# Kernel optimization log

Hardware: AMD Instinct MI355X
Metric: run time of the kernel (lower is better)

The kernel has to match this reference:

```python
import jax, jax.numpy as jnp
import numpy as np

B, S, D = 2, 2048, 1024
H = 16
HD = D // H
MLP = 4096
EPS = 1e-5


def _layernorm(x, g, b):
    mu = jnp.mean(x, axis=-1, keepdims=True)
    var = jnp.mean(jnp.square(x - mu), axis=-1, keepdims=True)
    return (x - mu) * jax.lax.rsqrt(var + EPS) * g + b


def setup_inputs() -> dict:
    key = jax.random.key(0)
    ks = jax.random.split(key, 16)
    sd = 0.02
    return {
        "x": jax.random.normal(ks[0], (B, S, D), jnp.float32),
        "dis_attn_mask": jax.random.normal(ks[1], (B, S, S), jnp.float32) * 0.1,
        "cls_attn_mask": jax.random.normal(ks[2], (B, S, S), jnp.float32) * 0.1,
        "wq": jax.random.normal(ks[3], (D, D), jnp.float32) * sd,
        "bq": jnp.zeros((D,), jnp.float32),
        "wk": jax.random.normal(ks[4], (D, D), jnp.float32) * sd,
        "bk": jnp.zeros((D,), jnp.float32),
        "wv": jax.random.normal(ks[5], (D, D), jnp.float32) * sd,
        "bv": jnp.zeros((D,), jnp.float32),
        "ln1_g": jnp.ones((D,), jnp.float32),
        "ln1_b": jnp.zeros((D,), jnp.float32),
        "ln2_g": jnp.ones((D,), jnp.float32),
        "ln2_b": jnp.zeros((D,), jnp.float32),
        "w1": jax.random.normal(ks[6], (D, MLP), jnp.float32) * sd,
        "b1": jnp.zeros((MLP,), jnp.float32),
        "w2": jax.random.normal(ks[7], (MLP, D), jnp.float32) * sd,
        "b2": jnp.zeros((D,), jnp.float32),
    }


def reference(x, dis_attn_mask, cls_attn_mask, wq, bq, wk, bk, wv, bv,
              ln1_g, ln1_b, ln2_g, ln2_b, w1, b1, w2, b2):
    res = x
    h = _layernorm(x, ln1_g, ln1_b)
    q = h @ wq + bq
    k = h @ wk + bk
    v = h @ wv + bv
    # NOTE: original torch code uses .view(B, H, S, HD) on a contiguous
    # [B, S, D] tensor (no transpose); row-major reshape reproduces this.
    q = q.reshape(B, H, S, HD)
    k = k.reshape(B, H, S, HD)
    v = v.reshape(B, H, S, HD)
    w = jnp.einsum('bhsd,bhtd->bhst', q, k) * (HD ** -0.5)
    w = w + dis_attn_mask[:, None] + cls_attn_mask[:, None]
    w = jax.nn.softmax(w, axis=-1)
    h_attn = jnp.einsum('bhst,bhtd->bhsd', w, v).reshape(B, S, D)
    h = h_attn + res
    h = _layernorm(h, ln2_g, ln2_b)
    res2 = h
    h = jax.nn.gelu(h @ w1 + b1, approximate=False) @ w2 + b2
    return h + res2
```

## Files before the change

kernel.cpp:

```cpp
#include <hip/hip_runtime.h>
#include <hip/hip_bf16.h>
#include <math.h>

#define BB 2
#define SS 2048
#define DD 1024
#define HH 16
#define MLPD 4096

typedef __attribute__((ext_vector_type(8))) short bf16x8;
typedef __attribute__((ext_vector_type(4))) float f32x4;
typedef __attribute__((ext_vector_type(4))) unsigned short us4;

static __device__ __forceinline__ float fast_exp2(float x) {
#if __has_builtin(__builtin_amdgcn_exp2f)
  return __builtin_amdgcn_exp2f(x);
#else
  return exp2f(x);
#endif
}
static __device__ __forceinline__ float fast_rcp(float x) {
#if __has_builtin(__builtin_amdgcn_rcpf)
  return __builtin_amdgcn_rcpf(x);
#else
  return 1.0f / x;
#endif
}

static __device__ __forceinline__ unsigned short f2bf(float f) {
  union { float f; unsigned int u; } v; v.f = f;
  unsigned int r = v.u + 0x7fffu + ((v.u >> 16) & 1u);
  return (unsigned short)(r >> 16);
}
static __device__ __forceinline__ float bf2f(unsigned short b) {
  return __uint_as_float(((unsigned int)b) << 16);
}

static __device__ __forceinline__ float gelu_f(float x) {
  float u = x * x;
  float z = x * fmaf(u, 0.0713548162f, 1.59576912f);
  float e = fast_exp2(z * -1.44269504f);
  return x * fast_rcp(1.0f + e);
}

static __device__ __forceinline__ int swz(int row) {
  return (row & 3) ^ ((row >> 2) & 3);
}

static __device__ __forceinline__ void async16(const unsigned short* g, unsigned short* l) {
  __builtin_amdgcn_global_load_lds(
      (const __attribute__((address_space(1))) unsigned int*)g,
      (__attribute__((address_space(3))) unsigned int*)l, 16, 0, 0);
}

__global__ __launch_bounds__(256) void transpose_to_bf16(
    const float* __restrict__ src, unsigned short* __restrict__ dst,
    int K, int N) {
  __shared__ float tile[32][33];
  int t = threadIdx.x;
  int c = t & 31, rl = t >> 5;
  int bx = blockIdx.x, by = blockIdx.y;
#pragma unroll
  for (int i = 0; i < 4; ++i) {
    int row = rl * 4 + i;
    tile[row][c] = src[(size_t)(by * 32 + row) * N + bx * 32 + c];
  }
  __syncthreads();
#pragma unroll
  for (int i = 0; i < 4; ++i) {
    int n = rl * 4 + i;
    dst[(size_t)(bx * 32 + n) * K + by * 32 + c] = f2bf(tile[c][n]);
  }
}

__global__ __launch_bounds__(256) void transpose_qkv(
    const float* __restrict__ wq, const float* __restrict__ wk,
    const float* __restrict__ wv, unsigned short* __restrict__ dst) {
  __shared__ float tile[32][33];
  const float* src = blockIdx.z == 0 ? wq : blockIdx.z == 1 ? wk : wv;
  unsigned short* d = dst + (size_t)blockIdx.z * 1024 * 1024;
  int t = threadIdx.x;
  int c = t & 31, rl = t >> 5;
  int bx = blockIdx.x, by = blockIdx.y;
#pragma unroll
  for (int i = 0; i < 4; ++i) {
    int row = rl * 4 + i;
    tile[row][c] = src[(size_t)(by * 32 + row) * DD + bx * 32 + c];
  }
  __syncthreads();
#pragma unroll
  for (int i = 0; i < 4; ++i) {
    int n = rl * 4 + i;
    d[(size_t)(bx * 32 + n) * DD + by * 32 + c] = f2bf(tile[c][n]);
  }
}

__global__ __launch_bounds__(256) void concat_bias(
    const float* __restrict__ bq, const float* __restrict__ bk,
    const float* __restrict__ bv, float* __restrict__ dst) {
  int i = blockIdx.x * 256 + threadIdx.x;
  if (i < 1024) dst[i] = bq[i];
  else if (i < 2048) dst[i] = bk[i - 1024];
  else if (i < 3072) dst[i] = bv[i - 2048];
}

__global__ __launch_bounds__(256) void mask_prep2(
    const float* __restrict__ dis, const float* __restrict__ cls,
    unsigned short* __restrict__ cmP) {
  int qt = blockIdx.x, wave = blockIdx.y, b = blockIdx.z;
  int tid = threadIdx.x;
  int ktg = tid >> 6, lane = tid & 63;
  int g = lane >> 4, c16 = lane & 15;
  const float* db = dis + (size_t)b * SS * SS;
  const float* cb = cls + (size_t)b * SS * SS;
  unsigned short* ob =
      cmP + ((((size_t)b * 16 + qt) * 8 + wave) * 32) * 64 * 16;
  int row0 = qt * 128 + wave * 16 + g * 4;
#pragma unroll
  for (int i = 0; i < 8; ++i) {
    int kt = ktg * 8 + i;
    int col0 = kt * 64 + c16;
    short v[16];
#pragma unroll
    for (int t = 0; t < 4; ++t)
#pragma unroll
      for (int r = 0; r < 4; ++r) {
        size_t idx = (size_t)(row0 + r) * SS + col0 + t * 16;
        v[t * 4 + r] = (short)f2bf((db[idx] + cb[idx]) * 8.0f);
      }
    unsigned short* o = ob + ((size_t)kt * 64 + lane) * 16;
    *(bf16x8*)(o) = *(bf16x8*)&v[0];
    *(bf16x8*)(o + 8) = *(bf16x8*)&v[8];
  }
}

template <bool BF_IN, bool ADD>
__global__ __launch_bounds__(256) void ln_bf16(
    const void* __restrict__ in, const float* __restrict__ add,
    const float* __restrict__ g, const float* __restrict__ beta,
    unsigned short* __restrict__ out) {
  int row = blockIdx.x;
  int t = threadIdx.x;
  float x[4];
  if (BF_IN) {
    us4 b4 = *(const us4*)((const unsigned short*)in + (size_t)row * DD + t * 4);
#pragma unroll
    for (int i = 0; i < 4; ++i) x[i] = bf2f(b4[i]);
  } else {
    float4 f4 = *(const float4*)((const float*)in + (size_t)row * DD + t * 4);
    x[0] = f4.x; x[1] = f4.y; x[2] = f4.z; x[3] = f4.w;
  }
  if (ADD) {
    float4 a4 = *(const float4*)(add + (size_t)row * DD + t * 4);
    x[0] += a4.x; x[1] += a4.y; x[2] += a4.z; x[3] += a4.w;
  }
  float s1 = x[0] + x[1] + x[2] + x[3];
  float s2 = x[0] * x[0] + x[1] * x[1] + x[2] * x[2] + x[3] * x[3];
#pragma unroll
  for (int off = 32; off > 0; off >>= 1) {
    s1 += __shfl_down(s1, off);
    s2 += __shfl_down(s2, off);
  }
  __shared__ float sa[4], sb[4];
  int wid = t >> 6;
  if ((t & 63) == 0) { sa[wid] = s1; sb[wid] = s2; }
  __syncthreads();
  s1 = sa[0] + sa[1] + sa[2] + sa[3];
  s2 = sb[0] + sb[1] + sb[2] + sb[3];
  float mean = s1 * (1.0f / 1024.0f);
  float var = s2 * (1.0f / 1024.0f) - mean * mean;
  float rstd = rsqrtf(var + 1e-5f);
  float4 gv = *(const float4*)(g + t * 4);
  float4 bv = *(const float4*)(beta + t * 4);
  us4 o;
  o[0] = f2bf((x[0] - mean) * rstd * gv.x + bv.x);
  o[1] = f2bf((x[1] - mean) * rstd * gv.y + bv.y);
  o[2] = f2bf((x[2] - mean) * rstd * gv.z + bv.z);
  o[3] = f2bf((x[3] - mean) * rstd * gv.w + bv.w);
  *(us4*)(out + (size_t)row * DD + t * 4) = o;
}

template <int BN, bool GELU, bool ADDSRC, bool OUT_BF16, bool SPLIT3>
__global__ __launch_bounds__(256) void gemm_bf16(
    const unsigned short* __restrict__ A, const unsigned short* __restrict__ BT,
    const float* __restrict__ bias, const unsigned short* __restrict__ addsrc,
    void* C0, void* C1, void* C2, int M, int N, int K) {
  constexpr int BJ = BN / 32;
  constexpr int BCH = BN / 64;
  __shared__ __align__(16) unsigned short As[128][32];
  __shared__ __align__(16) unsigned short Bs[BN][32];
  int tid = threadIdx.x;
  int wave = tid >> 6, lane = tid & 63;
  int g = lane >> 4, c16 = lane & 15;
  int m0 = blockIdx.y * 128, n0 = blockIdx.x * BN;
  int wm = (wave >> 1) * 64, wn = (wave & 1) * (BN / 2);
  int lrow = lane >> 2, lq = lane & 3;
  int dq = (lq ^ swz(lrow)) * 8;
  const unsigned short* aS = A + (size_t)(m0 + wave * 32 + lrow) * K + lq * 8;
  unsigned short* aD0 = &As[wave * 32 + lrow][dq];
  unsigned short* aD1 = &As[wave * 32 + 16 + lrow][dq];
  const unsigned short* bS = BT + (size_t)(n0 + wave * (BCH * 16) + lrow) * K + lq * 8;
  unsigned short* bD0 = &Bs[wave * (BCH * 16) + lrow][dq];
  unsigned short* bD1 = &Bs[(wave * (BCH * 16) + 16 + lrow) % BN][dq];
  int vA = (g ^ swz(c16)) * 8;
  const int KI = K / 32;
  const size_t rK = 16 * (size_t)K;

  bf16x8 a0a = *(const bf16x8*)(aS);
  bf16x8 a1a = *(const bf16x8*)(aS + rK);
  bf16x8 b0a = *(const bf16x8*)(bS);
  bf16x8 b1a;
  if constexpr (BCH == 2) b1a = *(const bf16x8*)(bS + rK);
  bf16x8 a0b = *(const bf16x8*)(aS + 32);
  bf16x8 a1b = *(const bf16x8*)(aS + rK + 32);
  bf16x8 b0b = *(const bf16x8*)(bS + 32);
  bf16x8 b1b;
  if constexpr (BCH == 2) b1b = *(const bf16x8*)(bS + rK + 32);

  f32x4 acc[4][BJ] = {};
  for (int kt = 0; kt < KI; kt += 2) {
    __syncthreads();
    *(bf16x8*)aD0 = a0a;
    *(bf16x8*)aD1 = a1a;
    *(bf16x8*)bD0 = b0a;
    if constexpr (BCH == 2) *(bf16x8*)bD1 = b1a;
    __syncthreads();
    if (kt + 2 < KI) {
      int ko = (kt + 2) * 32;
      a0a = *(const bf16x8*)(aS + ko);
      a1a = *(const bf16x8*)(aS + rK + ko);
      b0a = *(const bf16x8*)(bS + ko);
      if constexpr (BCH == 2) b1a = *(const bf16x8*)(bS + rK + ko);
    }
    {
      bf16x8 a[4], b[BJ];
#pragma unroll
      for (int i = 0; i < 4; ++i) a[i] = *(const bf16x8*)&As[wm + i * 16 + c16][vA];
#pragma unroll
      for (int j = 0; j < BJ; ++j) b[j] = *(const bf16x8*)&Bs[wn + j * 16 + c16][vA];
#pragma unroll
      for (int i = 0; i < 4; ++i)
#pragma unroll
        for (int j = 0; j < BJ; ++j)
          acc[i][j] = __builtin_amdgcn_mfma_f32_16x16x32_bf16(a[i], b[j], acc[i][j], 0, 0, 0);
    }
    __syncthreads();
    *(bf16x8*)aD0 = a0b;
    *(bf16x8*)aD1 = a1b;
    *(bf16x8*)bD0 = b0b;
    if constexpr (BCH == 2) *(bf16x8*)bD1 = b1b;
    __syncthreads();
    if (kt + 3 < KI) {
      int ko = (kt + 3) * 32;
      a0b = *(const bf16x8*)(aS + ko);
      a1b = *(const bf16x8*)(aS + rK + ko);
      b0b = *(const bf16x8*)(bS + ko);
      if constexpr (BCH == 2) b1b = *(const bf16x8*)(bS + rK + ko);
    }
    {
      bf16x8 a[4], b[BJ];
#pragma unroll
      for (int i = 0; i < 4; ++i) a[i] = *(const bf16x8*)&As[wm + i * 16 + c16][vA];
#pragma unroll
      for (int j = 0; j < BJ; ++j) b[j] = *(const bf16x8*)&Bs[wn + j * 16 + c16][vA];
#pragma unroll
      for (int i = 0; i < 4; ++i)
#pragma unroll
        for (int j = 0; j < BJ; ++j)
          acc[i][j] = __builtin_amdgcn_mfma_f32_16x16x32_bf16(a[i], b[j], acc[i][j], 0, 0, 0);
    }
  }
  unsigned short* dstb = nullptr;
  int lc0 = 0;
  if (SPLIT3) {
    int which = n0 >> 10;
    dstb = (unsigned short*)(which == 0 ? C0 : which == 1 ? C1 : C2);
    lc0 = n0 & 1023;
  }
#pragma unroll
  for (int j = 0; j < BJ; ++j) {
    int coff = wn + j * 16 + c16;
    float bj = bias[n0 + coff];
#pragma unroll
    for (int i = 0; i < 4; ++i) {
#pragma unroll
      for (int r = 0; r < 4; ++r) {
        int row = m0 + wm + i * 16 + g * 4 + r;
        float cval = acc[i][j][r] + bj;
        if (GELU) cval = gelu_f(cval);
        if (ADDSRC) cval += bf2f(addsrc[(size_t)row * N + n0 + coff]);
        if (SPLIT3) {
          dstb[(size_t)row * 1024 + lc0 + coff] = f2bf(cval);
        } else if (OUT_BF16) {
          ((unsigned short*)C0)[(size_t)row * N + n0 + coff] = f2bf(cval);
        } else {
          ((float*)C0)[(size_t)row * N + n0 + coff] = cval;
        }
      }
    }
  }
}

#define VMW(n) asm volatile("s_waitcnt vmcnt(" #n ")" ::: "memory")
#define BARX() do { asm volatile("" ::: "memory"); \
                    __builtin_amdgcn_s_barrier(); \
                    asm volatile("" ::: "memory"); } while (0)

template <bool GELU, bool SPLIT3>
__global__ __launch_bounds__(512, 2) void gemm256(
    const unsigned short* __restrict__ A, const unsigned short* __restrict__ BT,
    const float* __restrict__ bias, void* C0, void* C1, void* C2,
    int N, int K) {
  __shared__ __align__(16) char lds[2][2][2][16384];
  int tid = threadIdx.x;
  int lane = tid & 63, w = tid >> 6;
  int g = lane >> 4, c16 = lane & 15;
  int wm16 = (w >> 2) << 4;
  int wn16 = (w & 3) << 4;
  int m0 = blockIdx.y << 8, n0 = blockIdx.x << 8;

  int st0 = tid >> 6, ci0 = tid & 63;
  int cp0 = ci0 ^ (((ci0 >> 5) & 1) << 1);
  int sr0 = ((st0 >> 1) << 4) + (cp0 >> 2);
  int sk0 = ((st0 & 1) << 5) + ((cp0 & 3) << 3);
  size_t soff = (size_t)sr0 * K + sk0;

  auto stage = [&](int op, int h, int tt, int d) {
    const unsigned short* base = (op == 0 ? A : BT);
    int row0 = (op == 0 ? m0 : n0) + (h << 7);
    const unsigned short* src = base + (size_t)row0 * K + (tt << 6) + soff;
    unsigned short* dst = (unsigned short*)&lds[op][d][h][tid * 16];
    async16(src, dst);
    async16(src + ((size_t)K << 6), dst + 4096);
  };

  auto foff = [&](int r, int ke) -> int {
    int stt = ((r >> 4) << 1) + (ke >> 5);
    int loc = ((r & 15) << 6) + ((ke & 31) << 1);
    return (stt << 10) + (loc ^ (((r >> 3) & 1) << 5));
  };
  int offA[4][2], offB[2][2];
#pragma unroll
  for (int ii = 0; ii < 4; ++ii)
#pragma unroll
    for (int ks = 0; ks < 2; ++ks)
      offA[ii][ks] = foff(ii * 32 + wm16 + c16, ks * 32 + g * 8);
#pragma unroll
  for (int jj = 0; jj < 2; ++jj)
#pragma unroll
    for (int ks = 0; ks < 2; ++ks)
      offB[jj][ks] = foff(jj * 64 + wn16 + c16, ks * 32 + g * 8);

  f32x4 acc[8][4] = {};

#define MFMA_Q(IH, JH, AF, BF) do {                                           \
    __builtin_amdgcn_s_setprio(1);                                            \
    _Pragma("unroll") for (int ii = 0; ii < 4; ++ii)                          \
      _Pragma("unroll") for (int jj = 0; jj < 2; ++jj) {                      \
        acc[(IH)*4+ii][(JH)*2+jj] = __builtin_amdgcn_mfma_f32_16x16x32_bf16(  \
            AF[ii][0], BF[jj][0], acc[(IH)*4+ii][(JH)*2+jj], 0, 0, 0);        \
        acc[(IH)*4+ii][(JH)*2+jj] = __builtin_amdgcn_mfma_f32_16x16x32_bf16(  \
            AF[ii][1], BF[jj][1], acc[(IH)*4+ii][(JH)*2+jj], 0, 0, 0);        \
      }                                                                       \
    __builtin_amdgcn_s_setprio(0);                                            \
  } while (0)

  stage(0, 0, 0, 0);
  stage(1, 0, 0, 0);
  stage(0, 1, 0, 0);
  stage(1, 1, 0, 0);
  VMW(4);
  BARX();

  const int KT = K >> 6;
  for (int kt = 0; kt < KT; ++kt) {
    int d = kt & 1, dn = d ^ 1;
    int t1 = kt + 1 < KT ? kt + 1 : KT - 1;
    const char* pd = &lds[0][d][0][0];
    bf16x8 A0f[4][2], A1f[4][2], Bf[2][2];

#pragma unroll
    for (int ii = 0; ii < 4; ++ii)
#pragma unroll
      for (int ks = 0; ks < 2; ++ks)
        A0f[ii][ks] = *(const bf16x8*)(pd + offA[ii][ks]);
#pragma unroll
    for (int jj = 0; jj < 2; ++jj)
#pragma unroll
      for (int ks = 0; ks < 2; ++ks)
        Bf[jj][ks] = *(const bf16x8*)(pd + 65536 + offB[jj][ks]);
    stage(0, 0, t1, dn);
    VMW(4);
    BARX();
    MFMA_Q(0, 0, A0f, Bf);
    BARX();

#pragma unroll
    for (int ii = 0; ii < 4; ++ii)
#pragma unroll
      for (int ks = 0; ks < 2; ++ks)
        A1f[ii][ks] = *(const bf16x8*)(pd + 16384 + offA[ii][ks]);
    stage(1, 0, t1, dn);
    VMW(4);
    BARX();
    MFMA_Q(1, 0, A1f, Bf);
    BARX();

#pragma unroll
    for (int jj = 0; jj < 2; ++jj)
#pragma unroll
      for (int ks = 0; ks < 2; ++ks)
        Bf[jj][ks] = *(const bf16x8*)(pd + 81920 + offB[jj][ks]);
    stage(0, 1, t1, dn);
    VMW(4);
    BARX();
    MFMA_Q(1, 1, A1f, Bf);
    BARX();

    stage(1, 1, t1, dn);
    VMW(4);
    BARX();
    MFMA_Q(0, 1, A0f, Bf);
    BARX();
  }
#undef MFMA_Q
  VMW(0);

  unsigned short* dstb = nullptr;
  int lc0 = 0;
  if (SPLIT3) {
    int which = n0 >> 10;
    dstb = (unsigned short*)(which == 0 ? C0 : which == 1 ? C1 : C2);
    lc0 = n0 & 1023;
  }
#pragma unroll
  for (int i = 0; i < 8; ++i) {
#pragma unroll
    for (int j = 0; j < 4; ++j) {
      int row_b = m0 + ((i >> 2) << 7) + ((i & 3) << 5) + wm16 + (g << 2);
      int colp = ((j >> 1) << 7) + ((j & 1) << 6) + wn16 + c16;
      float bj = bias[n0 + colp];
#pragma unroll
      for (int r = 0; r < 4; ++r) {
        float cv = acc[i][j][r] + bj;
        if (GELU) cv = gelu_f(cv);
        int row = row_b + r;
        if (SPLIT3) {
          dstb[(size_t)row * 1024 + lc0 + colp] = f2bf(cv);
        } else {
          ((unsigned short*)C0)[(size_t)row * N + n0 + colp] = f2bf(cv);
        }
      }
    }
  }
}

__global__ __launch_bounds__(512) void attn_mfma(
    const unsigned short* __restrict__ q, const unsigned short* __restrict__ k,
    const unsigned short* __restrict__ v, const unsigned short* __restrict__ cmP,
    unsigned short* __restrict__ outO) {
  __shared__ __align__(16) unsigned short Ks[2][64][32];
  __shared__ __align__(16) unsigned short Vt[64][72];
  __shared__ __align__(16) unsigned short Ps[128][72];
  int tid = threadIdx.x;
  int wave = tid >> 6, lane = tid & 63;
  int g = lane >> 4, c16 = lane & 15;
  int qt = blockIdx.x, h = blockIdx.y, b = blockIdx.z;
  int s0 = qt * 128;
  int wr = wave * 16;
  size_t headoff = (size_t)b * SS * DD + (size_t)h * SS * 64;
  const unsigned short* qb = q + headoff;
  const unsigned short* kb = k + headoff;
  const unsigned short* vb = v + headoff;
  const unsigned short* csrc =
      cmP + ((((size_t)b * 16 + qt) * 8 + wave) * 32 * 64 + lane) * 16;

  int kkey = tid >> 3, kseg = tid & 7;
  unsigned short* kdst = &Ks[kseg >> 2][kkey][((kseg & 3) ^ swz(kkey)) * 8];
  const unsigned short* ksrc = kb + (size_t)kkey * 64 + kseg * 8;
  const unsigned short* vsrc = vb + (size_t)lane * 64 + wave * 8;
  int vK = (g ^ swz(c16)) * 8;

  bf16x8 qf0, qf1;
  {
    size_t qrow = (size_t)(s0 + wr + c16) * 64;
    qf0 = *(const bf16x8*)(qb + qrow + g * 8);
    qf1 = *(const bf16x8*)(qb + qrow + 32 + g * 8);
  }
  bf16x8 ones;
#pragma unroll
  for (int j = 0; j < 8; ++j) ones[j] = (short)0x3F80;
  f32x4 o[4] = {};
  f32x4 ol = {};
  const float scale2 = 0.18033688f;

  bf16x8 kreg = *(const bf16x8*)(ksrc);
  bf16x8 vreg = *(const bf16x8*)(vsrc);
  bf16x8 cmA = *(const bf16x8*)(csrc);
  bf16x8 cmB = *(const bf16x8*)(csrc + 8);

  for (int kt = 0; kt < 32; ++kt) {
    __syncthreads();
    *(bf16x8*)kdst = kreg;
#pragma unroll
    for (int j = 0; j < 8; ++j) Vt[wave * 8 + j][lane] = (unsigned short)vreg[j];
    __syncthreads();

    int ktn = kt + 1 < 32 ? kt + 1 : 31;
    bf16x8 kregN = *(const bf16x8*)(ksrc + (size_t)ktn * 4096);
    bf16x8 vregN = *(const bf16x8*)(vsrc + (size_t)ktn * 4096);
    bf16x8 cmAN = *(const bf16x8*)(csrc + (size_t)ktn * 1024);
    bf16x8 cmBN = *(const bf16x8*)(csrc + (size_t)ktn * 1024 + 8);

    f32x4 s[4];
#pragma unroll
    for (int r = 0; r < 4; ++r) {
      s[0][r] = bf2f((unsigned short)cmA[r]);
      s[1][r] = bf2f((unsigned short)cmA[4 + r]);
      s[2][r] = bf2f((unsigned short)cmB[r]);
      s[3][r] = bf2f((unsigned short)cmB[4 + r]);
    }
#pragma unroll
    for (int t = 0; t < 4; ++t) {
      bf16x8 b0 = *(const bf16x8*)&Ks[0][t * 16 + c16][vK];
      bf16x8 b1 = *(const bf16x8*)&Ks[1][t * 16 + c16][vK];
      s[t] = __builtin_amdgcn_mfma_f32_16x16x32_bf16(qf0, b0, s[t], 0, 0, 0);
      s[t] = __builtin_amdgcn_mfma_f32_16x16x32_bf16(qf1, b1, s[t], 0, 0, 0);
    }
#pragma unroll
    for (int t = 0; t < 4; ++t)
#pragma unroll
      for (int r = 0; r < 4; ++r) {
        float p = fast_exp2(s[t][r] * scale2);
        Ps[wr + g * 4 + r][t * 16 + c16] = (unsigned short)(__float_as_uint(p) >> 16);
      }
#pragma unroll
    for (int ks = 0; ks < 2; ++ks) {
      bf16x8 pa = *(const bf16x8*)&Ps[wr + c16][ks * 32 + g * 8];
#pragma unroll
      for (int t2 = 0; t2 < 4; ++t2) {
        bf16x8 vb8 = *(const bf16x8*)&Vt[t2 * 16 + c16][ks * 32 + g * 8];
        o[t2] = __builtin_amdgcn_mfma_f32_16x16x32_bf16(pa, vb8, o[t2], 0, 0, 0);
      }
      ol = __builtin_amdgcn_mfma_f32_16x16x32_bf16(pa, ones, ol, 0, 0, 0);
    }
    kreg = kregN;
    vreg = vregN;
    cmA = cmAN;
    cmB = cmBN;
  }
  float inv[4];
#pragma unroll
  for (int r = 0; r < 4; ++r) inv[r] = fast_rcp(ol[r]);
#pragma unroll
  for (int t2 = 0; t2 < 4; ++t2)
#pragma unroll
    for (int r = 0; r < 4; ++r) {
      int srow = s0 + wr + g * 4 + r;
      outO[headoff + (size_t)srow * 64 + t2 * 16 + c16] = f2bf(o[t2][r] * inv[r]);
    }
}

extern "C" void kernel_launch(void* const* d_in, const int* in_sizes, int n_in,
                              void* d_out, int out_size, void* d_ws, size_t ws_size,
                              hipStream_t stream) {
  const float* x    = (const float*)d_in[0];
  const float* dis  = (const float*)d_in[1];
  const float* cls  = (const float*)d_in[2];
  const float* wq   = (const float*)d_in[3];
  const float* bq   = (const float*)d_in[4];
  const float* wk   = (const float*)d_in[5];
  const float* bk   = (const float*)d_in[6];
  const float* wv   = (const float*)d_in[7];
  const float* bv   = (const float*)d_in[8];
  const float* ln1g = (const float*)d_in[9];
  const float* ln1b = (const float*)d_in[10];
  const float* ln2g = (const float*)d_in[11];
  const float* ln2b = (const float*)d_in[12];
  const float* w1   = (const float*)d_in[13];
  const float* b1   = (const float*)d_in[14];
  const float* w2   = (const float*)d_in[15];
  const float* b2   = (const float*)d_in[16];
  float* out = (float*)d_out;
  char* ws = (char*)d_ws;

  unsigned short* qkvwT = (unsigned short*)(ws + 0);
  unsigned short* w1T   = (unsigned short*)(ws + 6291456);
  unsigned short* w2T   = (unsigned short*)(ws + 14680064);
  float*          qkvb  = (float*)(ws + 23068672);
  unsigned short* r1    = (unsigned short*)(ws + 23134208);
  unsigned short* qbuf  = (unsigned short*)(ws + 31522816);
  unsigned short* kbuf  = (unsigned short*)(ws + 39911424);
  unsigned short* vbuf  = (unsigned short*)(ws + 48300032);
  unsigned short* h2    = (unsigned short*)(ws + 56688640);
  unsigned short* cmP   = (unsigned short*)(ws + 65077248);
  unsigned short* mm    = (unsigned short*)(ws + 23134208);
  unsigned short* h1 = r1;
  unsigned short* attnO = r1;

  const int rows = BB * SS;

  transpose_qkv<<<dim3(DD / 32, DD / 32, 3), 256, 0, stream>>>(wq, wk, wv, qkvwT);
  transpose_to_bf16<<<dim3(MLPD / 32, DD / 32), 256, 0, stream>>>(w1, w1T, DD, MLPD);
  transpose_to_bf16<<<dim3(DD / 32, MLPD / 32), 256, 0, stream>>>(w2, w2T, MLPD, DD);
  concat_bias<<<12, 256, 0, stream>>>(bq, bk, bv, qkvb);
  mask_prep2<<<dim3(SS / 128, 8, BB), 256, 0, stream>>>(dis, cls, cmP);

  ln_bf16<false, false><<<rows, 256, 0, stream>>>(x, nullptr, ln1g, ln1b, h1);

  gemm256<false, true><<<dim3(3072 / 256, rows / 256), 512, 0, stream>>>(
      h1, qkvwT, qkvb, qbuf, kbuf, vbuf, 3072, DD);

  attn_mfma<<<dim3(SS / 128, HH, BB), 512, 0, stream>>>(qbuf, kbuf, vbuf, cmP, attnO);

  ln_bf16<true, true><<<rows, 256, 0, stream>>>(attnO, x, ln2g, ln2b, h2);

  gemm256<true, false><<<dim3(MLPD / 256, rows / 256), 512, 0, stream>>>(
      h2, w1T, b1, mm, nullptr, nullptr, MLPD, DD);

  gemm_bf16<64, false, true, false, false><<<dim3(DD / 64, rows / 128), 256, 0, stream>>>(
      mm, w2T, b2, h2, out, nullptr, nullptr, rows, DD, MLPD);
}
```

Baseline: 412.3 us.

## Coalesce mask prep via LDS, swizzle GEMM tile order, split attention into smaller blocks

The mask preprocessing kernel now reads the dis/cls masks with float4 coalesced loads into shared memory and then scatters them into the MFMA fragment layout, instead of doing strided scalar global loads. The 256x256 GEMM remaps workgroup IDs into an XCD-aware order (stride by 8) to improve L2 locality. Attention moves from 128-row, 512-thread blocks to 64-row, 256-thread blocks, with each thread loading twice as much K/V, and is launched as two half-head launches. Together these aim to cut uncoalesced mask traffic and improve cache reuse and occupancy, at the cost of an extra kernel launch and K/V being reloaded by twice as many blocks.

```diff
diff --git a/kernel.cpp b/kernel.cpp
--- a/kernel.cpp
+++ b/kernel.cpp
@@ -104,31 +104,46 @@
   else if (i < 3072) dst[i] = bv[i - 2048];
 }
 
-__global__ __launch_bounds__(256) void mask_prep2(
+__global__ __launch_bounds__(256) void mask_prep3(
     const float* __restrict__ dis, const float* __restrict__ cls,
     unsigned short* __restrict__ cmP) {
-  int qt = blockIdx.x, wave = blockIdx.y, b = blockIdx.z;
-  int tid = threadIdx.x;
-  int ktg = tid >> 6, lane = tid & 63;
-  int g = lane >> 4, c16 = lane & 15;
+  __shared__ unsigned short sm[16][512];
+  int qtO = blockIdx.x, waveO = blockIdx.y;
+  int b = blockIdx.z >> 2, ktg = blockIdx.z & 3;
+  int t = threadIdx.x;
+  int row0 = qtO * 128 + waveO * 16;
+  int col0 = ktg * 512;
   const float* db = dis + (size_t)b * SS * SS;
   const float* cb = cls + (size_t)b * SS * SS;
+  int lrow = t >> 4, lcg = t & 15;
+#pragma unroll
+  for (int shot = 0; shot < 8; ++shot) {
+    int cc = lcg * 4 + shot * 64;
+    size_t idx = (size_t)(row0 + lrow) * SS + col0 + cc;
+    float4 d4 = *(const float4*)(db + idx);
+    float4 c4 = *(const float4*)(cb + idx);
+    us4 o;
+    o[0] = f2bf((d4.x + c4.x) * 8.0f);
+    o[1] = f2bf((d4.y + c4.y) * 8.0f);
+    o[2] = f2bf((d4.z + c4.z) * 8.0f);
+    o[3] = f2bf((d4.w + c4.w) * 8.0f);
+    *(us4*)&sm[lrow][cc] = o;
+  }
+  __syncthreads();
+  int ktL = t >> 5, lp = t & 31;
   unsigned short* ob =
-      cmP + ((((size_t)b * 16 + qt) * 8 + wave) * 32) * 64 * 16;
-  int row0 = qt * 128 + wave * 16 + g * 4;
-#pragma unroll
-  for (int i = 0; i < 8; ++i) {
-    int kt = ktg * 8 + i;
-    int col0 = kt * 64 + c16;
+      cmP + ((((size_t)b * 16 + qtO) * 8 + waveO) * 32 + ktg * 8 + ktL) * 64 * 16;
+#pragma unroll
+  for (int li = 0; li < 2; ++li) {
+    int l = lp * 2 + li;
+    int g = l >> 4, c16 = l & 15;
     short v[16];
 #pragma unroll
-    for (int t = 0; t < 4; ++t)
-#pragma unroll
-      for (int r = 0; r < 4; ++r) {
-        size_t idx = (size_t)(row0 + r) * SS + col0 + t * 16;
-        v[t * 4 + r] = (short)f2bf((db[idx] + cb[idx]) * 8.0f);
-      }
-    unsigned short* o = ob + ((size_t)kt * 64 + lane) * 16;
+    for (int t4 = 0; t4 < 4; ++t4)
+#pragma unroll
+      for (int r = 0; r < 4; ++r)
+        v[t4 * 4 + r] = (short)sm[g * 4 + r][ktL * 64 + t4 * 16 + c16];
+    unsigned short* o = ob + (size_t)l * 16;
     *(bf16x8*)(o) = *(bf16x8*)&v[0];
     *(bf16x8*)(o + 8) = *(bf16x8*)&v[8];
   }
@@ -317,7 +332,12 @@
   int g = lane >> 4, c16 = lane & 15;
   int wm16 = (w >> 2) << 4;
   int wn16 = (w & 3) << 4;
-  int m0 = blockIdx.y << 8, n0 = blockIdx.x << 8;
+  int nwg = gridDim.x * gridDim.y;
+  int wg = blockIdx.y * gridDim.x + blockIdx.x;
+  int cpx = nwg >> 3;
+  int sw = (wg & 7) * cpx + (wg >> 3);
+  int bx = sw % gridDim.x, by = sw / gridDim.x;
+  int m0 = by << 8, n0 = bx << 8;
 
   int st0 = tid >> 6, ci0 = tid & 63;
   int cp0 = ci0 ^ (((ci0 >> 5) & 1) << 1);
@@ -455,30 +475,35 @@
   }
 }
 
-__global__ __launch_bounds__(512) void attn_mfma(
+__global__ __launch_bounds__(256) void attn_mfma4(
     const unsigned short* __restrict__ q, const unsigned short* __restrict__ k,
     const unsigned short* __restrict__ v, const unsigned short* __restrict__ cmP,
-    unsigned short* __restrict__ outO) {
+    unsigned short* __restrict__ outO, int hbase) {
   __shared__ __align__(16) unsigned short Ks[2][64][32];
   __shared__ __align__(16) unsigned short Vt[64][72];
-  __shared__ __align__(16) unsigned short Ps[128][72];
+  __shared__ __align__(16) unsigned short Ps[64][72];
   int tid = threadIdx.x;
   int wave = tid >> 6, lane = tid & 63;
   int g = lane >> 4, c16 = lane & 15;
-  int qt = blockIdx.x, h = blockIdx.y, b = blockIdx.z;
-  int s0 = qt * 128;
+  int qt = blockIdx.x;
+  int h = hbase + blockIdx.y;
+  int b = blockIdx.z;
+  int s0 = qt * 64;
   int wr = wave * 16;
   size_t headoff = (size_t)b * SS * DD + (size_t)h * SS * 64;
   const unsigned short* qb = q + headoff;
   const unsigned short* kb = k + headoff;
   const unsigned short* vb = v + headoff;
+  int waveO = (qt & 1) * 4 + wave;
   const unsigned short* csrc =
-      cmP + ((((size_t)b * 16 + qt) * 8 + wave) * 32 * 64 + lane) * 16;
-
-  int kkey = tid >> 3, kseg = tid & 7;
-  unsigned short* kdst = &Ks[kseg >> 2][kkey][((kseg & 3) ^ swz(kkey)) * 8];
-  const unsigned short* ksrc = kb + (size_t)kkey * 64 + kseg * 8;
-  const unsigned short* vsrc = vb + (size_t)lane * 64 + wave * 8;
+      cmP + ((((size_t)b * 16 + (qt >> 1)) * 8 + waveO) * 32 * 64 + lane) * 16;
+
+  int kkey = tid >> 2, lq2 = tid & 3;
+  int ksg0 = lq2 * 2, ksg1 = lq2 * 2 + 1;
+  unsigned short* kdst0 = &Ks[ksg0 >> 2][kkey][((ksg0 & 3) ^ swz(kkey)) * 8];
+  unsigned short* kdst1 = &Ks[ksg1 >> 2][kkey][((ksg1 & 3) ^ swz(kkey)) * 8];
+  const unsigned short* ksrc = kb + (size_t)kkey * 64 + ksg0 * 8;
+  const unsigned short* vsrc = vb + (size_t)lane * 64 + wave * 16;
   int vK = (g ^ swz(c16)) * 8;
 
   bf16x8 qf0, qf1;
@@ -494,21 +519,29 @@
   f32x4 ol = {};
   const float scale2 = 0.18033688f;
 
-  bf16x8 kreg = *(const bf16x8*)(ksrc);
-  bf16x8 vreg = *(const bf16x8*)(vsrc);
+  bf16x8 kregA = *(const bf16x8*)(ksrc);
+  bf16x8 kregB = *(const bf16x8*)(ksrc + 8);
+  bf16x8 vregA = *(const bf16x8*)(vsrc);
+  bf16x8 vregB = *(const bf16x8*)(vsrc + 8);
   bf16x8 cmA = *(const bf16x8*)(csrc);
   bf16x8 cmB = *(const bf16x8*)(csrc + 8);
 
   for (int kt = 0; kt < 32; ++kt) {
     __syncthreads();
-    *(bf16x8*)kdst = kreg;
-#pragma unroll
-    for (int j = 0; j < 8; ++j) Vt[wave * 8 + j][lane] = (unsigned short)vreg[j];
+    *(bf16x8*)kdst0 = kregA;
+    *(bf16x8*)kdst1 = kregB;
+#pragma unroll
+    for (int j = 0; j < 8; ++j) {
+      Vt[wave * 16 + j][lane] = (unsigned short)vregA[j];
+      Vt[wave * 16 + 8 + j][lane] = (unsigned short)vregB[j];
+    }
     __syncthreads();
 
     int ktn = kt + 1 < 32 ? kt + 1 : 31;
-    bf16x8 kregN = *(const bf16x8*)(ksrc + (size_t)ktn * 4096);
-    bf16x8 vregN = *(const bf16x8*)(vsrc + (size_t)ktn * 4096);
+    bf16x8 kregAN = *(const bf16x8*)(ksrc + (size_t)ktn * 4096);
+    bf16x8 kregBN = *(const bf16x8*)(ksrc + (size_t)ktn * 4096 + 8);
+    bf16x8 vregAN = *(const bf16x8*)(vsrc + (size_t)ktn * 4096);
+    bf16x8 vregBN = *(const bf16x8*)(vsrc + (size_t)ktn * 4096 + 8);
     bf16x8 cmAN = *(const bf16x8*)(csrc + (size_t)ktn * 1024);
     bf16x8 cmBN = *(const bf16x8*)(csrc + (size_t)ktn * 1024 + 8);
 
@@ -544,10 +577,9 @@
       }
       ol = __builtin_amdgcn_mfma_f32_16x16x32_bf16(pa, ones, ol, 0, 0, 0);
     }
-    kreg = kregN;
-    vreg = vregN;
-    cmA = cmAN;
-    cmB = cmBN;
+    kregA = kregAN; kregB = kregBN;
+    vregA = vregAN; vregB = vregBN;
+    cmA = cmAN; cmB = cmBN;
   }
   float inv[4];
 #pragma unroll
@@ -604,14 +636,17 @@
   transpose_to_bf16<<<dim3(MLPD / 32, DD / 32), 256, 0, stream>>>(w1, w1T, DD, MLPD);
   transpose_to_bf16<<<dim3(DD / 32, MLPD / 32), 256, 0, stream>>>(w2, w2T, MLPD, DD);
   concat_bias<<<12, 256, 0, stream>>>(bq, bk, bv, qkvb);
-  mask_prep2<<<dim3(SS / 128, 8, BB), 256, 0, stream>>>(dis, cls, cmP);
+  mask_prep3<<<dim3(16, 8, 8), 256, 0, stream>>>(dis, cls, cmP);
 
   ln_bf16<false, false><<<rows, 256, 0, stream>>>(x, nullptr, ln1g, ln1b, h1);
 
   gemm256<false, true><<<dim3(3072 / 256, rows / 256), 512, 0, stream>>>(
       h1, qkvwT, qkvb, qbuf, kbuf, vbuf, 3072, DD);
 
-  attn_mfma<<<dim3(SS / 128, HH, BB), 512, 0, stream>>>(qbuf, kbuf, vbuf, cmP, attnO);
+  attn_mfma4<<<dim3(SS / 64, HH / 2, BB), 256, 0, stream>>>(
+      qbuf, kbuf, vbuf, cmP, attnO, 0);
+  attn_mfma4<<<dim3(SS / 64, HH / 2, BB), 256, 0, stream>>>(
+      qbuf, kbuf, vbuf, cmP, attnO, 8);
 
   ln_bf16<true, true><<<rows, 256, 0, stream>>>(attnO, x, ln2g, ln2b, h2);
 
```

Measured after the change: 428.2 us. 3.8% more time.

## Coalesce mask prep via LDS, swizzle GEMM block order, reschedule async stages

Applied to the files above, without the earlier changes.

The mask preparation kernel now reads dis/cls rows with coalesced float4 loads into shared memory and then scatters them into the MFMA-fragment layout from LDS, replacing strided scalar global reads. It also launches four times more blocks, each covering a quarter of the key columns. Both GEMM kernels remap block IDs with an XCD-aware swizzle (round-robin groups of 8) to improve L2 locality across chiplets. The 256x256 GEMM issues async stages earlier and waits less often to deepen prefetch overlap, which risks hazards if the vmcnt accounting is wrong.

```diff
diff --git a/kernel.cpp b/kernel.cpp
--- a/kernel.cpp
+++ b/kernel.cpp
@@ -104,31 +104,46 @@
   else if (i < 3072) dst[i] = bv[i - 2048];
 }
 
-__global__ __launch_bounds__(256) void mask_prep2(
+__global__ __launch_bounds__(256) void mask_prep3(
     const float* __restrict__ dis, const float* __restrict__ cls,
     unsigned short* __restrict__ cmP) {
-  int qt = blockIdx.x, wave = blockIdx.y, b = blockIdx.z;
-  int tid = threadIdx.x;
-  int ktg = tid >> 6, lane = tid & 63;
-  int g = lane >> 4, c16 = lane & 15;
+  __shared__ unsigned short sm[16][512];
+  int qtO = blockIdx.x, waveO = blockIdx.y;
+  int b = blockIdx.z >> 2, ktg = blockIdx.z & 3;
+  int t = threadIdx.x;
+  int row0 = qtO * 128 + waveO * 16;
+  int col0 = ktg * 512;
   const float* db = dis + (size_t)b * SS * SS;
   const float* cb = cls + (size_t)b * SS * SS;
+  int lrow = t >> 4, lcg = t & 15;
+#pragma unroll
+  for (int shot = 0; shot < 8; ++shot) {
+    int cc = lcg * 4 + shot * 64;
+    size_t idx = (size_t)(row0 + lrow) * SS + col0 + cc;
+    float4 d4 = *(const float4*)(db + idx);
+    float4 c4 = *(const float4*)(cb + idx);
+    us4 o;
+    o[0] = f2bf((d4.x + c4.x) * 8.0f);
+    o[1] = f2bf((d4.y + c4.y) * 8.0f);
+    o[2] = f2bf((d4.z + c4.z) * 8.0f);
+    o[3] = f2bf((d4.w + c4.w) * 8.0f);
+    *(us4*)&sm[lrow][cc] = o;
+  }
+  __syncthreads();
+  int ktL = t >> 5, lp = t & 31;
   unsigned short* ob =
-      cmP + ((((size_t)b * 16 + qt) * 8 + wave) * 32) * 64 * 16;
-  int row0 = qt * 128 + wave * 16 + g * 4;
-#pragma unroll
-  for (int i = 0; i < 8; ++i) {
-    int kt = ktg * 8 + i;
-    int col0 = kt * 64 + c16;
+      cmP + ((((size_t)b * 16 + qtO) * 8 + waveO) * 32 + ktg * 8 + ktL) * 64 * 16;
+#pragma unroll
+  for (int li = 0; li < 2; ++li) {
+    int l = lp * 2 + li;
+    int g = l >> 4, c16 = l & 15;
     short v[16];
 #pragma unroll
-    for (int t = 0; t < 4; ++t)
-#pragma unroll
-      for (int r = 0; r < 4; ++r) {
-        size_t idx = (size_t)(row0 + r) * SS + col0 + t * 16;
-        v[t * 4 + r] = (short)f2bf((db[idx] + cb[idx]) * 8.0f);
-      }
-    unsigned short* o = ob + ((size_t)kt * 64 + lane) * 16;
+    for (int t4 = 0; t4 < 4; ++t4)
+#pragma unroll
+      for (int r = 0; r < 4; ++r)
+        v[t4 * 4 + r] = (short)sm[g * 4 + r][ktL * 64 + t4 * 16 + c16];
+    unsigned short* o = ob + (size_t)l * 16;
     *(bf16x8*)(o) = *(bf16x8*)&v[0];
     *(bf16x8*)(o + 8) = *(bf16x8*)&v[8];
   }
@@ -192,7 +207,12 @@
   int tid = threadIdx.x;
   int wave = tid >> 6, lane = tid & 63;
   int g = lane >> 4, c16 = lane & 15;
-  int m0 = blockIdx.y * 128, n0 = blockIdx.x * BN;
+  int nwg = gridDim.x * gridDim.y;
+  int wg = blockIdx.y * gridDim.x + blockIdx.x;
+  int cpx = nwg >> 3;
+  int sw = (wg & 7) * cpx + (wg >> 3);
+  int bxs = sw % gridDim.x, bys = sw / gridDim.x;
+  int m0 = bys * 128, n0 = bxs * BN;
   int wm = (wave >> 1) * 64, wn = (wave & 1) * (BN / 2);
   int lrow = lane >> 2, lq = lane & 3;
   int dq = (lq ^ swz(lrow)) * 8;
@@ -317,7 +337,12 @@
   int g = lane >> 4, c16 = lane & 15;
   int wm16 = (w >> 2) << 4;
   int wn16 = (w & 3) << 4;
-  int m0 = blockIdx.y << 8, n0 = blockIdx.x << 8;
+  int nwg = gridDim.x * gridDim.y;
+  int wg = blockIdx.y * gridDim.x + blockIdx.x;
+  int cpx = nwg >> 3;
+  int sw = (wg & 7) * cpx + (wg >> 3);
+  int bx = sw % gridDim.x, by = sw / gridDim.x;
+  int m0 = by << 8, n0 = bx << 8;
 
   int st0 = tid >> 6, ci0 = tid & 63;
   int cp0 = ci0 ^ (((ci0 >> 5) & 1) << 1);
@@ -390,7 +415,8 @@
       for (int ks = 0; ks < 2; ++ks)
         Bf[jj][ks] = *(const bf16x8*)(pd + 65536 + offB[jj][ks]);
     stage(0, 0, t1, dn);
-    VMW(4);
+    stage(1, 0, t1, dn);
+    VMW(6);
     BARX();
     MFMA_Q(0, 0, A0f, Bf);
     BARX();
@@ -400,8 +426,8 @@
 #pragma unroll
       for (int ks = 0; ks < 2; ++ks)
         A1f[ii][ks] = *(const bf16x8*)(pd + 16384 + offA[ii][ks]);
-    stage(1, 0, t1, dn);
-    VMW(4);
+    stage(0, 1, t1, dn);
+    VMW(6);
     BARX();
     MFMA_Q(1, 0, A1f, Bf);
     BARX();
@@ -411,13 +437,11 @@
 #pragma unroll
       for (int ks = 0; ks < 2; ++ks)
         Bf[jj][ks] = *(const bf16x8*)(pd + 81920 + offB[jj][ks]);
-    stage(0, 1, t1, dn);
-    VMW(4);
+    stage(1, 1, t1, dn);
     BARX();
     MFMA_Q(1, 1, A1f, Bf);
     BARX();
 
-    stage(1, 1, t1, dn);
     VMW(4);
     BARX();
     MFMA_Q(0, 1, A0f, Bf);
@@ -604,7 +628,7 @@
   transpose_to_bf16<<<dim3(MLPD / 32, DD / 32), 256, 0, stream>>>(w1, w1T, DD, MLPD);
   transpose_to_bf16<<<dim3(DD / 32, MLPD / 32), 256, 0, stream>>>(w2, w2T, MLPD, DD);
   concat_bias<<<12, 256, 0, stream>>>(bq, bk, bv, qkvb);
-  mask_prep2<<<dim3(SS / 128, 8, BB), 256, 0, stream>>>(dis, cls, cmP);
+  mask_prep3<<<dim3(16, 8, 8), 256, 0, stream>>>(dis, cls, cmP);
 
   ln_bf16<false, false><<<rows, 256, 0, stream>>>(x, nullptr, ln1g, ln1b, h1);
 
```

Measured after the change: 389.8 us. -5.5%, faster.
